# Kernel optimization log

Measured on AMD Instinct MI355X. Metric: run time of the kernel, lower is better.

## Reference

```python
import jax, jax.numpy as jnp
import numpy as np

B, N, C, K, KS, OC = 8, 4096, 64, 20, 16, 64


def setup_inputs() -> dict:
    key = jax.random.key(0)
    ks = jax.random.split(key, 6)
    return {
        'x': jax.random.normal(ks[0], (B, 3, N), jnp.float32),
        'feature': jax.random.normal(ks[1], (B, C, N), jnp.float32),
        'kernals': jax.random.normal(ks[2], (3, KS), jnp.float32),
        'mlp_w': jax.random.normal(ks[3], (C, 7), jnp.float32) * 0.1,
        'mlp_b': jnp.zeros((C,), jnp.float32),
        'conv_w': jax.random.normal(ks[4], (OC, 2 * C * KS), jnp.float32) * 0.02,
        'conv_b': jnp.zeros((OC,), jnp.float32),
        'bn_gamma': jnp.ones((OC,), jnp.float32),
        'bn_beta': jnp.zeros((OC,), jnp.float32),
    }


def reference(x, feature, kernals, mlp_w, mlp_b, conv_w, conv_b, bn_gamma, bn_beta):
    b, _, n = x.shape
    c = feature.shape[1]
    ksz = kernals.shape[1]
    k = K
    # ---- knn on coords ----
    xt = jnp.swapaxes(x, 1, 2)                      # [B,N,3]
    inner = -2.0 * jnp.einsum('bnc,bmc->bnm', xt, xt)
    xx = jnp.sum(xt * xt, axis=-1)                  # [B,N]
    pd = -xx[:, :, None] - inner - xx[:, None, :]   # negative squared dist
    idx = jax.lax.top_k(pd, k)[1]                   # [B,N,K] nearest (incl. self)
    gather = jax.vmap(lambda pts, i: pts[i])        # per-batch gather
    # ---- geometric features ----
    x_sp = gather(xt, idx)                          # [B,N,K,3]
    x_rel = x_sp - x_sp[:, :, 0:1, :]               # [B,N,K,3]
    x_dis = jnp.linalg.norm(x_rel, axis=-1, keepdims=True)
    center = jnp.broadcast_to(x_sp[:, :, 0:1, :], x_sp.shape)
    x_feats7 = jnp.concatenate([center, x_rel, x_dis], axis=-1)  # [B,N,K,7]
    # Conv1d(7,C,1) == pointwise linear over the 7 channels
    x_feats = jnp.einsum('bnkc,oc->bnok', x_feats7, mlp_w) + mlp_b[None, None, :, None]  # [B,N,C,K]
    # ---- neighbor feature gather ----
    ft = jnp.swapaxes(feature, 1, 2)                # [B,N,C]
    sp_f = gather(ft, idx)                          # [B,N,K,C]
    spirals = jnp.concatenate([jnp.swapaxes(sp_f, 2, 3), x_feats], axis=2)  # [B,N,2C,K]
    # ---- adjacency weights ----
    one_pad = jnp.zeros((k, ksz), jnp.float32).at[0, 0].set(1.0)
    aw = jnp.einsum('bnkc,cs->bnks', x_rel, kernals) + one_pad   # [B,N,K,KS]
    aw = jnp.where(aw > 0, aw, 0.0)
    aw = aw / (jnp.sum(aw, axis=2, keepdims=True) + 1e-6)
    aw = aw * aw
    aw = aw / (jnp.sum(aw, axis=2, keepdims=True) + 1e-6)
    aw = jnp.where(aw > 0.1, aw, 0.0)
    # ---- weighted aggregation + linear ----
    agg = jnp.einsum('bnck,bnks->bncs', spirals, aw)             # [B,N,2C,KS]
    agg = agg.reshape(b, n, 2 * c * ksz)
    out = agg @ conv_w.T + conv_b                                # [B,N,OC]
    out = jnp.swapaxes(out, 1, 2)                                # [B,OC,N]
    # ---- BatchNorm1d (training-mode batch statistics, eps=1e-5) ----
    mean = jnp.mean(out, axis=(0, 2), keepdims=True)
    var = jnp.var(out, axis=(0, 2), keepdims=True)
    out = (out - mean) / jnp.sqrt(var + 1e-5)
    out = out * bn_gamma[None, :, None] + bn_beta[None, :, None]
    return out
```

## Files before the change

kernel.cpp:

```cpp
#include <hip/hip_runtime.h>
#include <cfloat>
#include <math.h>

#define NB 8
#define NPT 4096
#define NC 64
#define KNN 20
#define KSZ 16
#define BPTS 8

typedef __attribute__((ext_vector_type(8))) short short8;
typedef __attribute__((ext_vector_type(4))) float f32x4;

__device__ __forceinline__ unsigned short f2bf(float f) {
  unsigned u = __float_as_uint(f);
  unsigned r = (u + 0x7fffu + ((u >> 16) & 1u)) >> 16;
  return (unsigned short)r;
}
__device__ __forceinline__ float bf2f(unsigned short h) {
  return __uint_as_float(((unsigned)h) << 16);
}

__global__ void k_pack_cw(const float* __restrict__ cw, unsigned short* __restrict__ bp) {
  int t = blockIdx.x * 256 + threadIdx.x;
  int j = t & 7, lane = (t >> 3) & 63, nt = (t >> 9) & 3, ks = t >> 11;
  int k = ks * 32 + ((lane >> 4) << 3) + j;
  int o = nt * 16 + (lane & 15);
  bp[t] = f2bf(cw[o * 2048 + k]);
}

__global__ void k_pack_cw2(const float* __restrict__ cw, const float* __restrict__ mlp_w,
                           const float* __restrict__ mlp_b, unsigned short* __restrict__ bp2) {
  int t = blockIdx.x * 256 + threadIdx.x;
  int jj = t & 7, lane = (t >> 3) & 63, nt = (t >> 9) & 3, ks2 = t >> 11;
  int k = ks2 * 32 + ((lane >> 4) << 3) + jj;
  int s = k >> 3, j = k & 7;
  int o = nt * 16 + (lane & 15);
  float acc = 0.0f;
  for (int c = 0; c < 64; ++c) {
    float coef = (j < 7) ? mlp_w[c * 7 + j] : mlp_b[c];
    acc = fmaf(cw[o * 2048 + 1024 + c * 16 + s], coef, acc);
  }
  bp2[t] = f2bf(acc);
}

__global__ void k_transpose_ft(const float* __restrict__ f, unsigned short* __restrict__ ft) {
  __shared__ float tile[64][65];
  int b = blockIdx.x >> 6;
  int n0 = (blockIdx.x & 63) * 64;
  int lane = threadIdx.x & 63;
  int rr = threadIdx.x >> 6;
#pragma unroll
  for (int c0 = 0; c0 < 64; c0 += 4) {
    int c = c0 + rr;
    tile[c][lane] = f[(b * 64 + c) * 4096 + n0 + lane];
  }
  __syncthreads();
#pragma unroll
  for (int m0 = 0; m0 < 64; m0 += 4) {
    int nn = m0 + rr;
    ft[(b * 4096 + n0 + nn) * 64 + lane] = f2bf(tile[lane][nn]);
  }
}

__device__ __noinline__ void knn_full(const float4* __restrict__ pts, int n, int lane,
                                      int g, int* __restrict__ idxOut) {
  const int M = 24;
  float4 qp = pts[n];
  float qx = qp.x, qy = qp.y, qz = qp.z;
  float v[M];
  int id[M];
#pragma unroll
  for (int r = 0; r < M; ++r) { v[r] = FLT_MAX; id[r] = 0x7fffffff; }
  for (int i = 0; i < 64; ++i) {
    int j = (i << 6) | lane;
    float4 p = pts[j];
    float dx = p.x - qx, dy = p.y - qy, dz = p.z - qz;
    float d2 = fmaf(dx, dx, fmaf(dy, dy, dz * dz));
    bool c[M];
#pragma unroll
    for (int r = 0; r < M; ++r) c[r] = d2 < v[r];
#pragma unroll
    for (int r = M - 1; r >= 1; --r) {
      v[r] = c[r - 1] ? v[r - 1] : (c[r] ? d2 : v[r]);
      id[r] = c[r - 1] ? id[r - 1] : (c[r] ? j : id[r]);
    }
    v[0] = c[0] ? d2 : v[0];
    id[0] = c[0] ? j : id[0];
  }
  unsigned long long key = ((unsigned long long)__float_as_uint(v[0]) << 32) | (unsigned)id[0];
  unsigned long long ext = ~0ull;
  for (int r = 0; r < 24; ++r) {
    unsigned long long k = key;
#pragma unroll
    for (int s = 1; s < 64; s <<= 1) {
      unsigned long long o = __shfl_xor(k, s, 64);
      k = (o < k) ? o : k;
    }
    if (lane == r) ext = k;
    if (key == k) {
#pragma unroll
      for (int q = 0; q < M - 1; ++q) { v[q] = v[q + 1]; id[q] = id[q + 1]; }
      v[M - 1] = FLT_MAX;
      id[M - 1] = 0x7fffffff;
      key = ((unsigned long long)__float_as_uint(v[0]) << 32) | (unsigned)id[0];
    }
  }
  int ei = (int)(unsigned)(ext & 0xffffffffu);
  bool al = lane < 24;
  double dv = -1.0;
  if (al) {
    float4 p = pts[ei];
    double dx = (double)p.x - (double)qx;
    double dy = (double)p.y - (double)qy;
    double dz = (double)p.z - (double)qz;
    dv = dx * dx + dy * dy + dz * dz;
  }
#pragma unroll
  for (int r = 0; r < 4; ++r) {
    double bd = al ? dv : -1.0;
    int bi = al ? ei : -1;
#pragma unroll
    for (int s = 1; s < 64; s <<= 1) {
      double od = __shfl_xor(bd, s, 64);
      int oi = __shfl_xor(bi, s, 64);
      if (od > bd || (od == bd && oi > bi)) { bd = od; bi = oi; }
    }
    if (al && ei == bi) al = false;
  }
  unsigned long long msk = __ballot(al && ei != n);
  if (al) {
    if (ei == n) {
      idxOut[g * 20] = n;
    } else {
      int pos = 1 + __popcll(msk & ((1ull << lane) - 1ull));
      idxOut[g * 20 + pos] = ei;
    }
  }
}

__launch_bounds__(1024, 2)
__global__ void k_knn(const float* __restrict__ x, int* __restrict__ idxOut) {
  __shared__ float4 pts[4096];
  int b = blockIdx.x >> 6;
  const float* xb = x + b * 3 * 4096;
  for (int i = threadIdx.x; i < 4096; i += 1024) {
    float px = xb[i], py = xb[4096 + i], pz = xb[8192 + i];
    pts[i] = make_float4(px, py, pz, fmaf(px, px, fmaf(py, py, pz * pz)));
  }
  __syncthreads();

  int lane = threadIdx.x & 63;
  int w = threadIdx.x >> 6;
  int nb = ((blockIdx.x & 63) << 6) + (w << 2);
  int gb = b * 4096 + nb;

  float m2x[4], m2y[4], m2z[4];
#pragma unroll
  for (int r = 0; r < 4; ++r) {
    float4 q = pts[nb + r];
    m2x[r] = -2.0f * q.x;
    m2y[r] = -2.0f * q.y;
    m2z[r] = -2.0f * q.z;
  }

  float v[4];
#pragma unroll
  for (int r = 0; r < 4; ++r) v[r] = FLT_MAX;
#pragma unroll 2
  for (int i = 0; i < 64; ++i) {
    float4 p = pts[(i << 6) | lane];
#pragma unroll
    for (int r = 0; r < 4; ++r) {
      float d = fmaf(m2z[r], p.z, fmaf(m2y[r], p.y, fmaf(m2x[r], p.x, p.w)));
      v[r] = fminf(v[r], d);
    }
  }

#pragma unroll
  for (int k = 2; k <= 64; k <<= 1) {
#pragma unroll
    for (int j = k >> 1; j > 0; j >>= 1) {
      bool sel = ((lane & k) == 0) == ((lane & j) == 0);
#pragma unroll
      for (int r = 0; r < 4; ++r) {
        float o = __shfl_xor(v[r], j, 64);
        float mn = fminf(v[r], o), mx = fmaxf(v[r], o);
        v[r] = sel ? mn : mx;
      }
    }
  }
  float T[4];
#pragma unroll
  for (int r = 0; r < 4; ++r) T[r] = __shfl(v[r], 23, 64);

  int ei[4], base[4];
  bool ovf[4];
#pragma unroll
  for (int r = 0; r < 4; ++r) { ei[r] = -1; base[r] = 0; ovf[r] = false; }
#pragma unroll 2
  for (int i = 0; i < 64; ++i) {
    float4 p = pts[(i << 6) | lane];
#pragma unroll
    for (int r = 0; r < 4; ++r) {
      float d = fmaf(m2z[r], p.z, fmaf(m2y[r], p.y, fmaf(m2x[r], p.x, p.w)));
      bool pred = (d <= T[r]);
      unsigned long long mask = __ballot(pred);
      if (mask) {
        int cnt = __popcll(mask);
        if (base[r] + cnt > 63) {
          ovf[r] = true;
        } else {
          int dst = pred ? (base[r] + __popcll(mask & ((1ull << lane) - 1ull))) : 63;
          int got = __builtin_amdgcn_ds_permute(dst << 2, (i << 6) | lane);
          bool recv = (lane >= base[r]) && (lane < base[r] + cnt);
          ei[r] = recv ? got : ei[r];
        }
        base[r] += cnt;
      }
    }
  }

#pragma unroll
  for (int r = 0; r < 4; ++r) {
    int n = nb + r, g = gb + r;
    bool ok = !ovf[r];
    if (ok) {
      float4 qp = pts[n];
      bool act = lane < base[r];
      int e = ei[r];
      double dm = 1e300;
      if (act) {
        float4 p = pts[e];
        double dx = (double)p.x - (double)qp.x;
        double dy = (double)p.y - (double)qp.y;
        double dz = (double)p.z - (double)qp.z;
        dm = dx * dx + dy * dy + dz * dz;
      }
      int rank = 0;
      for (int r2 = 0; r2 < base[r]; ++r2) {
        double dr = __shfl(dm, r2, 64);
        int ir = __shfl(e, r2, 64);
        bool less = (dr < dm) || (dr == dm && ir < e);
        rank += less ? 1 : 0;
      }
      bool keep = act && (rank < 20);
      bool isSelf = keep && (e == n);
      unsigned long long smask = __ballot(isSelf);
      ok = (smask != 0ull);
      if (ok) {
        if (isSelf) idxOut[g * 20] = n;
        unsigned long long msk = __ballot(keep && !isSelf);
        if (keep && !isSelf) {
          int pos = 1 + __popcll(msk & ((1ull << lane) - 1ull));
          idxOut[g * 20 + pos] = e;
        }
      }
    }
    if (!ok) knn_full(pts, n, lane, g, idxOut);
  }
}

#define AGG_OFF 0
#define AWB_OFF 16384
#define FPA_OFF 24576
#define F7S_OFF 28672
#define QL_OFF  31232
#define IDX_OFF 31360
#define SMEM_SZ 33792

__launch_bounds__(256, 4)
__global__ void k_main(const float* __restrict__ x, const float* __restrict__ feat,
                       const unsigned short* __restrict__ ftT, int useFtT,
                       const float* __restrict__ kern,
                       const unsigned short* __restrict__ bpk,
                       const unsigned short* __restrict__ bpk2,
                       const float* __restrict__ conv_b, const int* __restrict__ idxIn,
                       float* __restrict__ out) {
  __shared__ __align__(16) unsigned char smem[SMEM_SZ];
  unsigned short* agg = (unsigned short*)(smem + AGG_OFF);
  unsigned short* awB = (unsigned short*)(smem + AWB_OFF);
  float4* f7s = (float4*)(smem + F7S_OFF);
  float4* qL = (float4*)(smem + QL_OFF);
  int* idxL = (int*)(smem + IDX_OFF);

  int t = threadIdx.x;
  int lane = t & 63;
  int w = t >> 6;
  int b = blockIdx.x & 7;
  int n0 = (blockIdx.x >> 3) * BPTS;
  int g0 = b * 4096 + n0;
  const float* xb = x + b * 3 * 4096;

  {
    int pt = t >> 5, slot = t & 31;
    int n = n0 + pt;
    float qx = xb[n], qy = xb[4096 + n], qz = xb[8192 + n];
    if (slot < 20) {
      int kk = idxIn[(g0 + pt) * 20 + slot];
      idxL[pt * 20 + slot] = kk;
      float rx = xb[kk] - qx, ry = xb[4096 + kk] - qy, rz = xb[8192 + kk] - qz;
      float ds = sqrtf(rx * rx + ry * ry + rz * rz);
      f7s[pt * 20 + slot] = make_float4(rx, ry, rz, ds);
    } else if (slot == 20) {
      qL[pt] = make_float4(qx, qy, qz, 0.0f);
    }
  }
  __syncthreads();

  if (t < 128) {
    int pt = t >> 4, s = t & 15;
    float kx = kern[s], ky = kern[16 + s], kz = kern[32 + s];
    float wv[20];
#pragma unroll
    for (int k = 0; k < 20; ++k) {
      float4 f = f7s[pt * 20 + k];
      float dot = f.x * kx + f.y * ky + f.z * kz;
      if (s == 0 && k == 0) dot += 1.0f;
      wv[k] = dot > 0.0f ? dot : 0.0f;
    }
    float sum = 0.0f;
#pragma unroll
    for (int k = 0; k < 20; ++k) sum += wv[k];
    float inv1 = 1.0f / (sum + 1e-6f);
    float sum2 = 0.0f;
#pragma unroll
    for (int k = 0; k < 20; ++k) {
      float u = wv[k] * inv1;
      sum2 += u * u;
    }
    float inv2 = 1.0f / (sum2 + 1e-6f);
    float colsum = 0.0f;
    float F0 = 0.0f, F1 = 0.0f, F2 = 0.0f, F3 = 0.0f;
    unsigned short* awp = awB + pt * 512;
#pragma unroll
    for (int k = 0; k < 20; ++k) {
      float u = wv[k] * inv1;
      u = u * u * inv2;
      u = (u > 0.1f) ? u : 0.0f;
      awp[(((k >> 3) * 16 + s) << 3) + (k & 7)] = f2bf(u);
      colsum += u;
      float4 f = f7s[pt * 20 + k];
      F0 = fmaf(f.x, u, F0);
      F1 = fmaf(f.y, u, F1);
      F2 = fmaf(f.z, u, F2);
      F3 = fmaf(f.w, u, F3);
    }
#pragma unroll
    for (int k = 20; k < 32; ++k)
      awp[(((k >> 3) * 16 + s) << 3) + (k & 7)] = 0;
    float4 q = qL[pt];
    __align__(16) unsigned short tmp[8];
    tmp[0] = f2bf(q.x * colsum);
    tmp[1] = f2bf(q.y * colsum);
    tmp[2] = f2bf(q.z * colsum);
    tmp[3] = f2bf(F0);
    tmp[4] = f2bf(F1);
    tmp[5] = f2bf(F2);
    tmp[6] = f2bf(F3);
    tmp[7] = f2bf(colsum);
    *(uint4*)(smem + FPA_OFF + pt * 256 + ((s ^ (pt & 7)) << 4)) = *(uint4*)tmp;
  }
  __syncthreads();

  {
    int r15 = lane & 15, chunk = lane >> 4;
#pragma unroll
    for (int half = 0; half < 2; ++half) {
      int pt = (w << 1) + half;
      int nofs[8];
#pragma unroll
      for (int j = 0; j < 8; ++j) {
        int k = (chunk << 3) + j;
        nofs[j] = (k < 20) ? ((b * 4096 + idxL[pt * 20 + k]) << 6) : -1;
      }
      short8 bfrag = *(const short8*)(awB + pt * 512 + (lane << 3));
      f32x4 accA[4];
#pragma unroll
      for (int ct = 0; ct < 4; ++ct) accA[ct] = (f32x4){0.f, 0.f, 0.f, 0.f};
#pragma unroll
      for (int ct = 0; ct < 4; ++ct) {
        int c = (ct << 4) + r15;
        union { short8 v; unsigned short u[8]; } af;
#pragma unroll
        for (int j = 0; j < 8; ++j) {
          unsigned short val = 0;
          if (nofs[j] >= 0) {
            if (useFtT) val = ftT[nofs[j] + c];
            else val = f2bf(feat[(b * 64 + c) * 4096 + (nofs[j] >> 6) - b * 4096]);
          }
          af.u[j] = val;
        }
        accA[ct] = __builtin_amdgcn_mfma_f32_16x16x32_bf16(af.v, bfrag, accA[ct], 0, 0, 0);
      }
      char* rb = (char*)(smem + AGG_OFF) + pt * 2048;
      int sw = (pt & 7) << 4;
#pragma unroll
      for (int ct = 0; ct < 4; ++ct)
#pragma unroll
        for (int q = 0; q < 4; ++q) {
          int kidx = (((ct << 4) + (chunk << 2) + q) << 4) + r15;
          *(unsigned short*)(rb + ((kidx << 1) ^ sw)) = f2bf(accA[ct][q]);
        }
    }
  }
  __syncthreads();

  f32x4 acc[4];
#pragma unroll
  for (int nt = 0; nt < 4; ++nt) acc[nt] = (f32x4){0.f, 0.f, 0.f, 0.f};
  {
    int r = lane & 15;
    const char* rowbase = (const char*)(smem + AGG_OFF) + r * 2048;
#pragma unroll
    for (int ks = 0; ks < 8; ++ks) {
      int ksl = w * 8 + ks;
      int off = (ksl * 64 + ((lane >> 4) << 4)) ^ ((r & 7) << 4);
      short8 af = *(const short8*)(rowbase + off);
#pragma unroll
      for (int nt = 0; nt < 4; ++nt) {
        short8 bf = *(const short8*)(bpk + (((ksl * 4 + nt) * 64 + lane) << 3));
        acc[nt] = __builtin_amdgcn_mfma_f32_16x16x32_bf16(af, bf, acc[nt], 0, 0, 0);
      }
    }
    {
      int chunk = (w << 2) + (lane >> 4);
      short8 af = *(const short8*)(smem + FPA_OFF + r * 256 + ((chunk ^ (r & 7)) << 4));
#pragma unroll
      for (int nt = 0; nt < 4; ++nt) {
        short8 bf = *(const short8*)(bpk2 + ((((w << 2) + nt) * 64 + lane) << 3));
        acc[nt] = __builtin_amdgcn_mfma_f32_16x16x32_bf16(af, bf, acc[nt], 0, 0, 0);
      }
    }
  }
  __syncthreads();

  float* red = (float*)(smem + AGG_OFF);
  {
#pragma unroll
    for (int nt = 0; nt < 4; ++nt)
#pragma unroll
      for (int r = 0; r < 4; ++r) {
        int row = ((lane >> 4) << 2) + r;
        if (row < 8) {
          int o = nt * 16 + (lane & 15);
          red[(w * 8 + row) * 64 + (o ^ ((row & 7) << 2))] = acc[nt][r];
        }
      }
  }
  __syncthreads();
#pragma unroll
  for (int rep = 0; rep < 2; ++rep) {
    int u = rep * 256 + t;
    int pt = u & 7, o = u >> 3;
    float s = conv_b[o];
#pragma unroll
    for (int w2 = 0; w2 < 4; ++w2) s += red[(w2 * 8 + pt) * 64 + (o ^ ((pt & 7) << 2))];
    out[(b * 64 + o) * 4096 + n0 + pt] = s;
  }
}

__global__ void k_bnstats1(const float* __restrict__ out, double* __restrict__ partial) {
  __shared__ double rs[256], rq[256];
  int o = blockIdx.x & 63, b = blockIdx.x >> 6;
  const float* p = out + (b * 64 + o) * 4096;
  double s = 0.0, q = 0.0;
  for (int i = threadIdx.x; i < 4096; i += 256) {
    double v = (double)p[i];
    s += v;
    q += v * v;
  }
  rs[threadIdx.x] = s;
  rq[threadIdx.x] = q;
  __syncthreads();
  for (int st = 128; st > 0; st >>= 1) {
    if ((int)threadIdx.x < st) {
      rs[threadIdx.x] += rs[threadIdx.x + st];
      rq[threadIdx.x] += rq[threadIdx.x + st];
    }
    __syncthreads();
  }
  if (threadIdx.x == 0) {
    partial[(o * 8 + b) * 2] = rs[0];
    partial[(o * 8 + b) * 2 + 1] = rq[0];
  }
}

__global__ void k_bnstats2(const double* __restrict__ partial, const float* __restrict__ gamma,
                           const float* __restrict__ beta, float* __restrict__ stats) {
  int o = threadIdx.x;
  double s = 0.0, q = 0.0;
#pragma unroll
  for (int b = 0; b < 8; ++b) {
    s += partial[(o * 8 + b) * 2];
    q += partial[(o * 8 + b) * 2 + 1];
  }
  double mean = s / 32768.0;
  double var = q / 32768.0 - mean * mean;
  double inv = 1.0 / sqrt(var + 1e-5);
  double sc = (double)gamma[o] * inv;
  stats[o * 2] = (float)sc;
  stats[o * 2 + 1] = (float)((double)beta[o] - mean * sc);
}

__global__ void k_bnapply(float* __restrict__ out, const float* __restrict__ stats) {
  int i4 = blockIdx.x * 256 + threadIdx.x;
  int o = (i4 >> 10) & 63;
  float sc = stats[o * 2], sh = stats[o * 2 + 1];
  float4 v = ((const float4*)out)[i4];
  v.x = fmaf(v.x, sc, sh);
  v.y = fmaf(v.y, sc, sh);
  v.z = fmaf(v.z, sc, sh);
  v.w = fmaf(v.w, sc, sh);
  ((float4*)out)[i4] = v;
}

extern "C" void kernel_launch(void* const* d_in, const int* in_sizes, int n_in,
                              void* d_out, int out_size, void* d_ws, size_t ws_size,
                              hipStream_t stream) {
  const float* x = (const float*)d_in[0];
  const float* feat = (const float*)d_in[1];
  const float* kern = (const float*)d_in[2];
  const float* mlp_w = (const float*)d_in[3];
  const float* mlp_b = (const float*)d_in[4];
  const float* conv_w = (const float*)d_in[5];
  const float* conv_b = (const float*)d_in[6];
  const float* gamma = (const float*)d_in[7];
  const float* beta = (const float*)d_in[8];
  float* out = (float*)d_out;
  char* ws = (char*)d_ws;

  int* idx = (int*)ws;
  double* partial = (double*)(ws + 2621440);
  float* stats = (float*)(ws + 2629632);
  unsigned short* bpk = (unsigned short*)(ws + 2633728);
  unsigned short* bpk2 = (unsigned short*)(ws + 2764800);
  unsigned short* ftT = (unsigned short*)(ws + 2781184);
  int useFtT = (ws_size >= (size_t)(2781184 + 4194304)) ? 1 : 0;

  k_pack_cw<<<256, 256, 0, stream>>>(conv_w, bpk);
  k_pack_cw2<<<32, 256, 0, stream>>>(conv_w, mlp_w, mlp_b, bpk2);
  if (useFtT) k_transpose_ft<<<512, 256, 0, stream>>>(feat, ftT);
  k_knn<<<512, 1024, 0, stream>>>(x, idx);
  k_main<<<4096, 256, 0, stream>>>(x, feat, ftT, useFtT, kern, bpk, bpk2,
                                   conv_b, idx, out);
  k_bnstats1<<<512, 256, 0, stream>>>(out, partial);
  k_bnstats2<<<1, 64, 0, stream>>>(partial, gamma, beta, stats);
  k_bnapply<<<2048, 256, 0, stream>>>(out, stats);
}
```

Measured before the change: 178.0 us.

## Restructure kNN candidate selection with packed FMA, half-sort threshold and LDS lists

The kNN kernel now computes distances for query pairs with packed v_pk_fma_f32 instructions. Its threshold comes from two 32-lane bitonic sorts (the max of each half's 12th smallest) instead of a full 64-lane sort. Candidates are gathered into per-row LDS lists with atomics rather than wave-wide ballot and ds_permute compaction. Ranking uses readlane over the candidate list, and results are written directly at their rank position. This cuts the sort and ballot work, at the cost of a looser threshold that admits more candidates, LDS atomic contention, and a fallback to the full kNN path when a list overflows 48 entries.

New measurement: 287.5 us. 61.6% more time.

```diff
diff --git a/kernel.cpp b/kernel.cpp
--- a/kernel.cpp
+++ b/kernel.cpp
@@ -11,6 +11,7 @@
 
 typedef __attribute__((ext_vector_type(8))) short short8;
 typedef __attribute__((ext_vector_type(4))) float f32x4;
+typedef __attribute__((ext_vector_type(2))) float f32x2;
 
 __device__ __forceinline__ unsigned short f2bf(float f) {
   unsigned u = __float_as_uint(f);
@@ -19,6 +20,25 @@
 }
 __device__ __forceinline__ float bf2f(unsigned short h) {
   return __uint_as_float(((unsigned)h) << 16);
+}
+
+__device__ __forceinline__ f32x2 pk_fma_zw(f32x2 a, f32x2 zw) {
+  f32x2 d;
+  asm("v_pk_fma_f32 %0, %1, %2, %2 op_sel:[0,0,1] op_sel_hi:[1,0,1]"
+      : "=v"(d) : "v"(a), "v"(zw));
+  return d;
+}
+__device__ __forceinline__ f32x2 pk_fma_s1hi(f32x2 a, f32x2 b, f32x2 c) {
+  f32x2 d;
+  asm("v_pk_fma_f32 %0, %1, %2, %3 op_sel:[0,1,0] op_sel_hi:[1,1,1]"
+      : "=v"(d) : "v"(a), "v"(b), "v"(c));
+  return d;
+}
+__device__ __forceinline__ f32x2 pk_fma_s1lo(f32x2 a, f32x2 b, f32x2 c) {
+  f32x2 d;
+  asm("v_pk_fma_f32 %0, %1, %2, %3 op_sel:[0,0,0] op_sel_hi:[1,0,1]"
+      : "=v"(d) : "v"(a), "v"(b), "v"(c));
+  return d;
 }
 
 __global__ void k_pack_cw(const float* __restrict__ cw, unsigned short* __restrict__ bp) {
@@ -63,6 +83,7 @@
   }
 }
 
+
 __device__ __noinline__ void knn_full(const float4* __restrict__ pts, int n, int lane,
                                       int g, int* __restrict__ idxOut) {
   const int M = 24;
@@ -142,8 +163,11 @@
 __launch_bounds__(1024, 2)
 __global__ void k_knn(const float* __restrict__ x, int* __restrict__ idxOut) {
   __shared__ float4 pts[4096];
+  __shared__ int cntL[64];
+  __shared__ unsigned short listL[64 * 48];
   int b = blockIdx.x >> 6;
   const float* xb = x + b * 3 * 4096;
+  if (threadIdx.x < 64) cntL[threadIdx.x] = 0;
   for (int i = threadIdx.x; i < 4096; i += 1024) {
     float px = xb[i], py = xb[4096 + i], pz = xb[8192 + i];
     pts[i] = make_float4(px, py, pz, fmaf(px, px, fmaf(py, py, pz * pz)));
@@ -152,112 +176,134 @@
 
   int lane = threadIdx.x & 63;
   int w = threadIdx.x >> 6;
-  int nb = ((blockIdx.x & 63) << 6) + (w << 2);
+  int row = w << 2;
+  int nb = ((blockIdx.x & 63) << 6) + row;
   int gb = b * 4096 + nb;
 
-  float m2x[4], m2y[4], m2z[4];
-#pragma unroll
-  for (int r = 0; r < 4; ++r) {
-    float4 q = pts[nb + r];
-    m2x[r] = -2.0f * q.x;
-    m2y[r] = -2.0f * q.y;
-    m2z[r] = -2.0f * q.z;
-  }
-
-  float v[4];
-#pragma unroll
-  for (int r = 0; r < 4; ++r) v[r] = FLT_MAX;
+  float4 q0 = pts[nb], q1 = pts[nb + 1], q2 = pts[nb + 2], q3 = pts[nb + 3];
+  f32x2 m2x01 = {-2.0f * q0.x, -2.0f * q1.x};
+  f32x2 m2y01 = {-2.0f * q0.y, -2.0f * q1.y};
+  f32x2 m2z01 = {-2.0f * q0.z, -2.0f * q1.z};
+  f32x2 m2x23 = {-2.0f * q2.x, -2.0f * q3.x};
+  f32x2 m2y23 = {-2.0f * q2.y, -2.0f * q3.y};
+  f32x2 m2z23 = {-2.0f * q2.z, -2.0f * q3.z};
+
+  float v0 = FLT_MAX, v1 = FLT_MAX, v2 = FLT_MAX, v3 = FLT_MAX;
+#pragma unroll 4
+  for (int i = 0; i < 64; ++i) {
+    float4 p = pts[(i << 6) | lane];
+    f32x2 pxy = {p.x, p.y}, pzw = {p.z, p.w};
+    f32x2 t0 = pk_fma_zw(m2z01, pzw);
+    f32x2 t1 = pk_fma_zw(m2z23, pzw);
+    t0 = pk_fma_s1hi(m2y01, pxy, t0);
+    t1 = pk_fma_s1hi(m2y23, pxy, t1);
+    t0 = pk_fma_s1lo(m2x01, pxy, t0);
+    t1 = pk_fma_s1lo(m2x23, pxy, t1);
+    v0 = fminf(v0, t0[0]);
+    v1 = fminf(v1, t0[1]);
+    v2 = fminf(v2, t1[0]);
+    v3 = fminf(v3, t1[1]);
+  }
+
+#pragma unroll
+  for (int k = 2; k <= 32; k <<= 1) {
+#pragma unroll
+    for (int j = k >> 1; j > 0; j >>= 1) {
+      bool sel = ((lane & k) == 0) == ((lane & j) == 0);
+      {
+        float o = __shfl_xor(v0, j, 64);
+        v0 = sel ? fminf(v0, o) : fmaxf(v0, o);
+      }
+      {
+        float o = __shfl_xor(v1, j, 64);
+        v1 = sel ? fminf(v1, o) : fmaxf(v1, o);
+      }
+      {
+        float o = __shfl_xor(v2, j, 64);
+        v2 = sel ? fminf(v2, o) : fmaxf(v2, o);
+      }
+      {
+        float o = __shfl_xor(v3, j, 64);
+        v3 = sel ? fminf(v3, o) : fmaxf(v3, o);
+      }
+    }
+  }
+  float T0 = fmaxf(__shfl(v0, 11, 64), __shfl(v0, 52, 64));
+  float T1 = fmaxf(__shfl(v1, 11, 64), __shfl(v1, 52, 64));
+  float T2 = fmaxf(__shfl(v2, 11, 64), __shfl(v2, 52, 64));
+  float T3 = fmaxf(__shfl(v3, 11, 64), __shfl(v3, 52, 64));
+
 #pragma unroll 2
   for (int i = 0; i < 64; ++i) {
-    float4 p = pts[(i << 6) | lane];
+    int j = (i << 6) | lane;
+    float4 p = pts[j];
+    f32x2 pxy = {p.x, p.y}, pzw = {p.z, p.w};
+    f32x2 t0 = pk_fma_zw(m2z01, pzw);
+    f32x2 t1 = pk_fma_zw(m2z23, pzw);
+    t0 = pk_fma_s1hi(m2y01, pxy, t0);
+    t1 = pk_fma_s1hi(m2y23, pxy, t1);
+    t0 = pk_fma_s1lo(m2x01, pxy, t0);
+    t1 = pk_fma_s1lo(m2x23, pxy, t1);
+    if (t0[0] <= T0) {
+      int s = atomicAdd(&cntL[row], 1);
+      if (s < 48) listL[row * 48 + s] = (unsigned short)j;
+    }
+    if (t0[1] <= T1) {
+      int s = atomicAdd(&cntL[row + 1], 1);
+      if (s < 48) listL[(row + 1) * 48 + s] = (unsigned short)j;
+    }
+    if (t1[0] <= T2) {
+      int s = atomicAdd(&cntL[row + 2], 1);
+      if (s < 48) listL[(row + 2) * 48 + s] = (unsigned short)j;
+    }
+    if (t1[1] <= T3) {
+      int s = atomicAdd(&cntL[row + 3], 1);
+      if (s < 48) listL[(row + 3) * 48 + s] = (unsigned short)j;
+    }
+  }
+
+  int c[4], e[4];
+  int rank0 = 0, rank1 = 0, rank2 = 0, rank3 = 0;
+  double dm[4];
+#pragma unroll
+  for (int r = 0; r < 4; ++r) {
+    int craw = cntL[row + r];
+    c[r] = (craw > 48) ? 0 : craw;
+    int e_ = (lane < c[r]) ? (int)listL[(row + r) * 48 + lane] : 0;
+    e[r] = e_;
+    float4 pp = pts[e_];
+    float4 qq = pts[nb + r];
+    double dx = (double)pp.x - (double)qq.x;
+    double dy = (double)pp.y - (double)qq.y;
+    double dz = (double)pp.z - (double)qq.z;
+    dm[r] = dx * dx + dy * dy + dz * dz;
+  }
+  int cmax = max(max(c[0], c[1]), max(c[2], c[3]));
+  for (int it = 0; it < cmax; ++it) {
 #pragma unroll
     for (int r = 0; r < 4; ++r) {
-      float d = fmaf(m2z[r], p.z, fmaf(m2y[r], p.y, fmaf(m2x[r], p.x, p.w)));
-      v[r] = fminf(v[r], d);
-    }
-  }
-
-#pragma unroll
-  for (int k = 2; k <= 64; k <<= 1) {
-#pragma unroll
-    for (int j = k >> 1; j > 0; j >>= 1) {
-      bool sel = ((lane & k) == 0) == ((lane & j) == 0);
-#pragma unroll
-      for (int r = 0; r < 4; ++r) {
-        float o = __shfl_xor(v[r], j, 64);
-        float mn = fminf(v[r], o), mx = fmaxf(v[r], o);
-        v[r] = sel ? mn : mx;
-      }
-    }
-  }
-  float T[4];
-#pragma unroll
-  for (int r = 0; r < 4; ++r) T[r] = __shfl(v[r], 23, 64);
-
-  int ei[4], base[4];
-  bool ovf[4];
-#pragma unroll
-  for (int r = 0; r < 4; ++r) { ei[r] = -1; base[r] = 0; ovf[r] = false; }
-#pragma unroll 2
-  for (int i = 0; i < 64; ++i) {
-    float4 p = pts[(i << 6) | lane];
-#pragma unroll
-    for (int r = 0; r < 4; ++r) {
-      float d = fmaf(m2z[r], p.z, fmaf(m2y[r], p.y, fmaf(m2x[r], p.x, p.w)));
-      bool pred = (d <= T[r]);
-      unsigned long long mask = __ballot(pred);
-      if (mask) {
-        int cnt = __popcll(mask);
-        if (base[r] + cnt > 63) {
-          ovf[r] = true;
-        } else {
-          int dst = pred ? (base[r] + __popcll(mask & ((1ull << lane) - 1ull))) : 63;
-          int got = __builtin_amdgcn_ds_permute(dst << 2, (i << 6) | lane);
-          bool recv = (lane >= base[r]) && (lane < base[r] + cnt);
-          ei[r] = recv ? got : ei[r];
-        }
-        base[r] += cnt;
-      }
-    }
-  }
-
+      int lo = __builtin_amdgcn_readlane(__double2loint(dm[r]), it);
+      int hi = __builtin_amdgcn_readlane(__double2hiint(dm[r]), it);
+      int ir = __builtin_amdgcn_readlane(e[r], it);
+      double dr = __hiloint2double(hi, lo);
+      bool less = (it < c[r]) && ((dr < dm[r]) || (dr == dm[r] && ir < e[r]));
+      int inc = (lane < c[r] && less) ? 1 : 0;
+      if (r == 0) rank0 += inc;
+      else if (r == 1) rank1 += inc;
+      else if (r == 2) rank2 += inc;
+      else rank3 += inc;
+    }
+  }
 #pragma unroll
   for (int r = 0; r < 4; ++r) {
-    int n = nb + r, g = gb + r;
-    bool ok = !ovf[r];
-    if (ok) {
-      float4 qp = pts[n];
-      bool act = lane < base[r];
-      int e = ei[r];
-      double dm = 1e300;
-      if (act) {
-        float4 p = pts[e];
-        double dx = (double)p.x - (double)qp.x;
-        double dy = (double)p.y - (double)qp.y;
-        double dz = (double)p.z - (double)qp.z;
-        dm = dx * dx + dy * dy + dz * dz;
-      }
-      int rank = 0;
-      for (int r2 = 0; r2 < base[r]; ++r2) {
-        double dr = __shfl(dm, r2, 64);
-        int ir = __shfl(e, r2, 64);
-        bool less = (dr < dm) || (dr == dm && ir < e);
-        rank += less ? 1 : 0;
-      }
-      bool keep = act && (rank < 20);
-      bool isSelf = keep && (e == n);
-      unsigned long long smask = __ballot(isSelf);
-      ok = (smask != 0ull);
-      if (ok) {
-        if (isSelf) idxOut[g * 20] = n;
-        unsigned long long msk = __ballot(keep && !isSelf);
-        if (keep && !isSelf) {
-          int pos = 1 + __popcll(msk & ((1ull << lane) - 1ull));
-          idxOut[g * 20 + pos] = e;
-        }
-      }
-    }
-    if (!ok) knn_full(pts, n, lane, g, idxOut);
+    int rk = (r == 0) ? rank0 : (r == 1) ? rank1 : (r == 2) ? rank2 : rank3;
+    bool kept = (lane < c[r]) && (rk < 20);
+    bool selfk = kept && (e[r] == nb + r);
+    if (__ballot(selfk) != 0ull) {
+      if (kept) idxOut[(gb + r) * 20 + rk] = e[r];
+    } else {
+      knn_full(pts, nb + r, lane, gb + r, idxOut);
+    }
   }
 }
 
```
